# Kernel tuning notes

Measured on AMD Instinct MI355X. Metric: run time of the kernel, lower is better.

The kernel has to match this reference:

```python
import jax, jax.numpy as jnp
import numpy as np
from jax import lax

T, IN, H, OUT = 8192, 1, 1024, 1


def setup_inputs() -> dict:
    key = jax.random.key(0)
    ks = jax.random.split(key, 7)
    s = 1.0 / np.sqrt(H)
    return {
        "x": jax.random.normal(ks[0], (T, IN), dtype=jnp.float32),
        "W_ih": jax.random.uniform(ks[1], (4 * H, IN), jnp.float32, -s, s),
        "W_hh": jax.random.uniform(ks[2], (4 * H, H), jnp.float32, -s, s),
        "b_ih": jax.random.uniform(ks[3], (4 * H,), jnp.float32, -s, s),
        "b_hh": jax.random.uniform(ks[4], (4 * H,), jnp.float32, -s, s),
        "W_fc": jax.random.uniform(ks[5], (OUT, H), jnp.float32, -s, s),
        "b_fc": jax.random.uniform(ks[6], (OUT,), jnp.float32, -s, s),
    }


def reference(x, W_ih, W_hh, b_ih, b_hh, W_fc, b_fc):
    # x: (T, input_size); batch dim of 1 is squeezed out.
    H_ = W_hh.shape[1]
    # Precompute input contribution to all gates for every timestep: (T, 4H)
    xg = x @ W_ih.T + (b_ih + b_hh)

    def step(carry, gx):
        h, c = carry
        g = gx + h @ W_hh.T  # (4H,) -- PyTorch gate order i, f, g, o
        i, f, gg, o = jnp.split(g, 4)
        c = jax.nn.sigmoid(f) * c + jax.nn.sigmoid(i) * jnp.tanh(gg)
        h = jax.nn.sigmoid(o) * jnp.tanh(c)
        return (h, c), h

    h0 = jnp.zeros((H_,), dtype=x.dtype)
    c0 = jnp.zeros((H_,), dtype=x.dtype)
    _, hs = lax.scan(step, (h0, c0), xg)  # hs: (T, H)
    return hs @ W_fc.T + b_fc  # (T, output_size)
```

## Files before the change

kernel.cpp:

```cpp
#include <hip/hip_runtime.h>

#define TT    8192
#define HD    1024
#define NBLK  256
#define NTHR  256
#define NBUF  4
#define NDR   8
#define RSTRIDE (NBUF * HD * 2)

typedef int i32x4 __attribute__((ext_vector_type(4)));
typedef int i32x2 __attribute__((ext_vector_type(2)));

__device__ __forceinline__ void llc_load_pair(const unsigned* p, i32x4& a, i32x4& b) {
  asm volatile("global_load_dwordx4 %0, %2, off sc0 sc1\n\t"
               "global_load_dwordx4 %1, %3, off sc0 sc1\n\t"
               "s_waitcnt vmcnt(0)"
               : "=&v"(a), "=&v"(b)
               : "v"(p), "v"(p + 4)
               : "memory");
}
__device__ __forceinline__ void llc_store2(unsigned* p, unsigned lo, unsigned hi) {
  i32x2 v; v.x = (int)lo; v.y = (int)hi;
  asm volatile("global_store_dwordx2 %0, %1, off sc0 sc1"
               :: "v"(p), "v"(v) : "memory");
}

__device__ __forceinline__ float sigf(float z) {
  return 1.0f / (1.0f + __expf(-z));
}
__device__ __forceinline__ float tanh_fast(float z) {
  float az = fabsf(z);
  float e  = __expf(2.0f * az);
  float t  = 1.0f - 2.0f / (e + 1.0f);
  return z < 0.0f ? -t : t;
}

#define FMA4(acc, hvv, wvv)                                      \
  acc = fmaf((hvv).x, (wvv).x, acc);                             \
  acc = fmaf((hvv).y, (wvv).y, acc);                             \
  acc = fmaf((hvv).z, (wvv).z, acc);                             \
  acc = fmaf((hvv).w, (wvv).w, acc);

extern "C" __global__ __launch_bounds__(NTHR, 1)
void lstm_persistent(const float* __restrict__ x,
                     const float* __restrict__ W_ih,
                     const float* __restrict__ W_hh,
                     const float* __restrict__ b_ih,
                     const float* __restrict__ b_hh,
                     const float* __restrict__ W_fc,
                     const float* __restrict__ b_fc,
                     float* __restrict__ out,
                     unsigned* __restrict__ hbufR)
{
  __shared__ float x_lds[TT];
  __shared__ float h_lds[HD];

  const int tid  = threadIdx.x;
  const int wave = tid >> 6;
  const int lane = tid & 63;
  const int g    = lane >> 4;
  const int kc   = lane & 15;
  const int blk  = blockIdx.x;
  const int unit = blk * 4 + wave;
  const unsigned myrep = (unsigned)(blk & (NDR - 1));

  for (int i = tid; i < TT / 4; i += NTHR)
    ((float4*)x_lds)[i] = ((const float4*)x)[i];

  float4 w4[16];
  {
    const float* wr = W_hh + (size_t)(g * HD + unit) * HD + kc * 4;
#pragma unroll
    for (int m = 0; m < 16; ++m)
      w4[m] = *((const float4*)(wr + m * 64));
  }
  float4 wfc4[4];
#pragma unroll
  for (int m = 0; m < 4; ++m)
    wfc4[m] = *((const float4*)(W_fc + m * 256 + lane * 4));
  const float bfc_val = b_fc[0];

  float wih_g[4], bs_g[4];
#pragma unroll
  for (int q = 0; q < 4; ++q) {
    int r = q * HD + unit;
    wih_g[q] = W_ih[r];
    bs_g[q]  = b_ih[r] + b_hh[r];
  }
  float c_state = 0.0f;
  __syncthreads();

  for (int t = 0; t < TT; ++t) {
    const bool doproj = (t > 0) && (wave == 1) && (blk == (t & 255));
    float accs = 0.0f;
    float4 hp4[4];

    if (t > 0) {
      const int slot = (t - 1) & (NBUF - 1);
      const unsigned* src =
          hbufR + myrep * RSTRIDE + ((size_t)slot * HD + tid * 4) * 2;
      i32x4 A, B;
      do {
        llc_load_pair(src, A, B);
      } while (!(A.y == t && A.w == t && B.y == t && B.w == t));
      float4 hv;
      hv.x = __int_as_float(A.x); hv.y = __int_as_float(A.z);
      hv.z = __int_as_float(B.x); hv.w = __int_as_float(B.z);
      ((float4*)h_lds)[tid] = hv;
      __syncthreads();

      const float* hp = h_lds + kc * 4;
      float s0 = 0.f, s1 = 0.f, s2 = 0.f, s3 = 0.f;
#pragma unroll
      for (int mb = 0; mb < 4; ++mb) {
        float4 ha = *((const float4*)(hp + (mb * 4 + 0) * 64));
        float4 hb = *((const float4*)(hp + (mb * 4 + 1) * 64));
        float4 hc = *((const float4*)(hp + (mb * 4 + 2) * 64));
        float4 hd = *((const float4*)(hp + (mb * 4 + 3) * 64));
        FMA4(s0, ha, w4[mb * 4 + 0]);
        FMA4(s1, hb, w4[mb * 4 + 1]);
        FMA4(s2, hc, w4[mb * 4 + 2]);
        FMA4(s3, hd, w4[mb * 4 + 3]);
      }
      accs = (s0 + s1) + (s2 + s3);

      if (doproj) {
#pragma unroll
        for (int m = 0; m < 4; ++m)
          hp4[m] = *((const float4*)(h_lds + m * 256 + lane * 4));
      }
    }

#pragma unroll
    for (int s = 1; s < 16; s <<= 1)
      accs += __shfl_xor(accs, s);

    float gi = __shfl(accs, 0);
    float gf = __shfl(accs, 16);
    float gg = __shfl(accs, 32);
    float go = __shfl(accs, 48);

    if (lane == 0) {
      float xt = x_lds[t];
      gi += fmaf(xt, wih_g[0], bs_g[0]);
      gf += fmaf(xt, wih_g[1], bs_g[1]);
      gg += fmaf(xt, wih_g[2], bs_g[2]);
      go += fmaf(xt, wih_g[3], bs_g[3]);
      c_state  = sigf(gf) * c_state + sigf(gi) * tanh_fast(gg);
      float hn = sigf(go) * tanh_fast(c_state);
      unsigned vv = __float_as_uint(hn), tg = (unsigned)(t + 1);
      unsigned* pb = hbufR + ((size_t)(t & (NBUF - 1)) * HD + unit) * 2;
#pragma unroll
      for (int r = 0; r < NDR; ++r)
        llc_store2(pb + r * RSTRIDE, vv, tg);
    }

    if (doproj) {
      float p = 0.f;
#pragma unroll
      for (int m = 0; m < 4; ++m) { FMA4(p, hp4[m], wfc4[m]); }
#pragma unroll
      for (int s = 1; s < 64; s <<= 1) p += __shfl_xor(p, s);
      if (lane == 0) out[t - 1] = p + bfc_val;
    }
  }

  if (blk == 0) {
    const unsigned* src =
        hbufR + (((size_t)((TT - 1) & (NBUF - 1)) * HD + tid * 4) * 2);
    i32x4 A, B;
    do {
      llc_load_pair(src, A, B);
    } while (!(A.y == TT && A.w == TT && B.y == TT && B.w == TT));
    float4 hv;
    hv.x = __int_as_float(A.x); hv.y = __int_as_float(A.z);
    hv.z = __int_as_float(B.x); hv.w = __int_as_float(B.z);
    ((float4*)h_lds)[tid] = hv;
    __syncthreads();
    if (wave == 1) {
      float p = 0.f;
#pragma unroll
      for (int m = 0; m < 4; ++m) {
        float4 hm = *((const float4*)(h_lds + m * 256 + lane * 4));
        FMA4(p, hm, wfc4[m]);
      }
#pragma unroll
      for (int s = 1; s < 64; s <<= 1) p += __shfl_xor(p, s);
      if (lane == 0) out[TT - 1] = p + bfc_val;
    }
  }
}

extern "C" void kernel_launch(void* const* d_in, const int* in_sizes, int n_in,
                              void* d_out, int out_size, void* d_ws, size_t ws_size,
                              hipStream_t stream) {
  const float* x   = (const float*)d_in[0];
  const float* Wih = (const float*)d_in[1];
  const float* Whh = (const float*)d_in[2];
  const float* bih = (const float*)d_in[3];
  const float* bhh = (const float*)d_in[4];
  const float* Wfc = (const float*)d_in[5];
  const float* bfc = (const float*)d_in[6];
  float* out = (float*)d_out;

  unsigned* hbufR = (unsigned*)d_ws;
  hipMemsetAsync(d_ws, 0, (size_t)NDR * RSTRIDE * sizeof(unsigned), stream);
  hipLaunchKernelGGL(lstm_persistent, dim3(NBLK), dim3(NTHR), 0, stream,
                     x, Wih, Whh, bih, bhh, Wfc, bfc, out, hbufR);
}
```

Before: 25.43 ms.

## Pack generation tag into low mantissa bits and drop replicated hidden-state buffers

Each hidden value now carries a 2-bit generation tag in its low mantissa bits, so a single dword replaces the value-plus-step pair. The eight replicated copies of the exchange buffer are removed, leaving one store per unit per step, and each poll becomes one dwordx4 load instead of two. This cuts exchange traffic and the per-step store count, but every block now polls the same buffer lines, which may create contention. It also gives up two mantissa bits of h and relies on a 0xAA memset to give initial tags that never match the expected generation.

```diff
diff --git a/kernel.cpp b/kernel.cpp
--- a/kernel.cpp
+++ b/kernel.cpp
@@ -5,23 +5,17 @@
 #define NBLK  256
 #define NTHR  256
 #define NBUF  4
-#define NDR   8
-#define RSTRIDE (NBUF * HD * 2)
 
 typedef int i32x4 __attribute__((ext_vector_type(4)));
-typedef int i32x2 __attribute__((ext_vector_type(2)));
-
-__device__ __forceinline__ void llc_load_pair(const unsigned* p, i32x4& a, i32x4& b) {
-  asm volatile("global_load_dwordx4 %0, %2, off sc0 sc1\n\t"
-               "global_load_dwordx4 %1, %3, off sc0 sc1\n\t"
-               "s_waitcnt vmcnt(0)"
-               : "=&v"(a), "=&v"(b)
-               : "v"(p), "v"(p + 4)
-               : "memory");
-}
-__device__ __forceinline__ void llc_store2(unsigned* p, unsigned lo, unsigned hi) {
-  i32x2 v; v.x = (int)lo; v.y = (int)hi;
-  asm volatile("global_store_dwordx2 %0, %1, off sc0 sc1"
+
+__device__ __forceinline__ i32x4 llc_load4i(const int* p) {
+  i32x4 r;
+  asm volatile("global_load_dwordx4 %0, %1, off sc0 sc1\n\ts_waitcnt vmcnt(0)"
+               : "=v"(r) : "v"(p) : "memory");
+  return r;
+}
+__device__ __forceinline__ void llc_store1u(unsigned* p, unsigned v) {
+  asm volatile("global_store_dword %0, %1, off sc0 sc1"
                :: "v"(p), "v"(v) : "memory");
 }
 
@@ -50,7 +44,7 @@
                      const float* __restrict__ W_fc,
                      const float* __restrict__ b_fc,
                      float* __restrict__ out,
-                     unsigned* __restrict__ hbufR)
+                     unsigned* __restrict__ vbuf)
 {
   __shared__ float x_lds[TT];
   __shared__ float h_lds[HD];
@@ -62,7 +56,6 @@
   const int kc   = lane & 15;
   const int blk  = blockIdx.x;
   const int unit = blk * 4 + wave;
-  const unsigned myrep = (unsigned)(blk & (NDR - 1));
 
   for (int i = tid; i < TT / 4; i += NTHR)
     ((float4*)x_lds)[i] = ((const float4*)x)[i];
@@ -97,15 +90,17 @@
 
     if (t > 0) {
       const int slot = (t - 1) & (NBUF - 1);
-      const unsigned* src =
-          hbufR + myrep * RSTRIDE + ((size_t)slot * HD + tid * 4) * 2;
-      i32x4 A, B;
+      const int gexp = ((t - 1) >> 2) & 3;
+      const int* src = (const int*)(vbuf + (size_t)slot * HD + tid * 4);
+      i32x4 V;
       do {
-        llc_load_pair(src, A, B);
-      } while (!(A.y == t && A.w == t && B.y == t && B.w == t));
+        V = llc_load4i(src);
+      } while ((((V.x ^ gexp) | (V.y ^ gexp) | (V.z ^ gexp) | (V.w ^ gexp)) & 3) != 0);
       float4 hv;
-      hv.x = __int_as_float(A.x); hv.y = __int_as_float(A.z);
-      hv.z = __int_as_float(B.x); hv.w = __int_as_float(B.z);
+      hv.x = __int_as_float(V.x & ~3);
+      hv.y = __int_as_float(V.y & ~3);
+      hv.z = __int_as_float(V.z & ~3);
+      hv.w = __int_as_float(V.w & ~3);
       ((float4*)h_lds)[tid] = hv;
       __syncthreads();
 
@@ -148,11 +143,8 @@
       go += fmaf(xt, wih_g[3], bs_g[3]);
       c_state  = sigf(gf) * c_state + sigf(gi) * tanh_fast(gg);
       float hn = sigf(go) * tanh_fast(c_state);
-      unsigned vv = __float_as_uint(hn), tg = (unsigned)(t + 1);
-      unsigned* pb = hbufR + ((size_t)(t & (NBUF - 1)) * HD + unit) * 2;
-#pragma unroll
-      for (int r = 0; r < NDR; ++r)
-        llc_store2(pb + r * RSTRIDE, vv, tg);
+      unsigned enc = (__float_as_uint(hn) & ~3u) | (unsigned)((t >> 2) & 3);
+      llc_store1u(vbuf + (size_t)(t & (NBUF - 1)) * HD + unit, enc);
     }
 
     if (doproj) {
@@ -166,15 +158,18 @@
   }
 
   if (blk == 0) {
-    const unsigned* src =
-        hbufR + (((size_t)((TT - 1) & (NBUF - 1)) * HD + tid * 4) * 2);
-    i32x4 A, B;
+    const int slot = (TT - 1) & (NBUF - 1);
+    const int gexp = ((TT - 1) >> 2) & 3;
+    const int* src = (const int*)(vbuf + (size_t)slot * HD + tid * 4);
+    i32x4 V;
     do {
-      llc_load_pair(src, A, B);
-    } while (!(A.y == TT && A.w == TT && B.y == TT && B.w == TT));
+      V = llc_load4i(src);
+    } while ((((V.x ^ gexp) | (V.y ^ gexp) | (V.z ^ gexp) | (V.w ^ gexp)) & 3) != 0);
     float4 hv;
-    hv.x = __int_as_float(A.x); hv.y = __int_as_float(A.z);
-    hv.z = __int_as_float(B.x); hv.w = __int_as_float(B.z);
+    hv.x = __int_as_float(V.x & ~3);
+    hv.y = __int_as_float(V.y & ~3);
+    hv.z = __int_as_float(V.z & ~3);
+    hv.w = __int_as_float(V.w & ~3);
     ((float4*)h_lds)[tid] = hv;
     __syncthreads();
     if (wave == 1) {
@@ -203,8 +198,8 @@
   const float* bfc = (const float*)d_in[6];
   float* out = (float*)d_out;
 
-  unsigned* hbufR = (unsigned*)d_ws;
-  hipMemsetAsync(d_ws, 0, (size_t)NDR * RSTRIDE * sizeof(unsigned), stream);
+  unsigned* vbuf = (unsigned*)d_ws;
+  hipMemsetAsync(d_ws, 0xAA, (size_t)NBUF * HD * sizeof(unsigned), stream);
   hipLaunchKernelGGL(lstm_persistent, dim3(NBLK), dim3(NTHR), 0, stream,
-                     x, Wih, Whh, bih, bhh, Wfc, bfc, out, hbufR);
-}
+                     x, Wih, Whh, bih, bhh, Wfc, bfc, out, vbuf);
+}
```

Result: slower. 33.53 ms (+31.9%).
